# Kernel tuning notes

Measured on AMD Instinct MI355X. Metric: run time of the kernel, lower is better.

The kernel has to match this reference:

```python
import jax, jax.numpy as jnp
import numpy as np
from jax import lax

EPS = 1e-20
BN_EPS = 1e-5
ATTN_SCALE = 2.8284271247461903  # sqrt(d_l=8)
NS = (32, 32, 32, 10)
DS = (8, 8, 8, 16)


def squash(x):
    # Efficient-CapsNet squash: (1 - 1/(exp(||x||)+eps)) * x/(||x||+eps)
    norm = jnp.linalg.norm(x, axis=-1, keepdims=True)
    return (1.0 - 1.0 / (jnp.exp(norm) + EPS)) * (x / (norm + EPS))


def conv2d(x, w, b, stride, groups=1):
    y = lax.conv_general_dilated(
        x, w, window_strides=(stride, stride), padding='VALID',
        dimension_numbers=('NCHW', 'OIHW', 'NCHW'),
        feature_group_count=groups)
    return y + b[None, :, None, None]


def bn(x, g, b, m, v):
    inv = g / jnp.sqrt(v + BN_EPS)
    return x * inv[None, :, None, None] + (b - m * inv)[None, :, None, None]


def fccaps(U_l, W):
    # U_l: (b, n_l, d_l), W: (n_l, n_h, d_l, d_h)
    U_hat = jnp.einsum('bij,ikjl->bikl', U_l, W)          # (b, n_l, n_h, d_h)
    A = jnp.einsum('bikl,bhkl->bhik', U_hat, U_hat)        # (b, n_l, n_l, n_h)
    A_sum = jnp.sum(A, axis=-2)                            # (b, n_l, n_h)
    C = jax.nn.softmax(A_sum / ATTN_SCALE, axis=-1)        # (b, n_l, n_h)
    U_h = jnp.einsum('bikl,bik->bkl', U_hat, C)            # (b, n_h, d_h)
    return squash(U_h)


def setup_inputs() -> dict:
    key = jax.random.key(0)
    ks = jax.random.split(key, 8)
    B = 512
    x = jax.random.normal(ks[0], (B, 1, 39, 39), dtype=jnp.float32)
    conv1_w = jax.random.normal(ks[1], (128, 1, 3, 3), jnp.float32) * 0.2
    conv1_b = jnp.zeros((128,), jnp.float32)
    conv2_w = jax.random.normal(ks[2], (256, 128, 3, 3), jnp.float32) * 0.04
    conv2_b = jnp.zeros((256,), jnp.float32)
    conv3_w = jax.random.normal(ks[3], (256, 1, 9, 9), jnp.float32) * 0.1  # depthwise
    conv3_b = jnp.zeros((256,), jnp.float32)
    bn1_g = jnp.ones((128,), jnp.float32); bn1_b = jnp.zeros((128,), jnp.float32)
    bn1_m = jnp.zeros((128,), jnp.float32); bn1_v = jnp.ones((128,), jnp.float32)
    bn2_g = jnp.ones((256,), jnp.float32); bn2_b = jnp.zeros((256,), jnp.float32)
    bn2_m = jnp.zeros((256,), jnp.float32); bn2_v = jnp.ones((256,), jnp.float32)
    # capsule weights, kaiming-ish scale sqrt(2/fan_in) with fan_in = n_h*d_l*d_h
    def caps_w(k, n_l, n_h, d_l, d_h):
        std = np.sqrt(2.0 / (n_h * d_l * d_h))
        return jax.random.normal(k, (n_l, n_h, d_l, d_h), jnp.float32) * std
    W1 = caps_w(ks[4], NS[0], NS[1], DS[0], DS[1])
    W2 = caps_w(ks[5], NS[1], NS[2], DS[1], DS[2])
    W3 = caps_w(ks[6], NS[2], NS[3], DS[2], DS[3])
    return dict(x=x, conv1_w=conv1_w, conv1_b=conv1_b,
                bn1_g=bn1_g, bn1_b=bn1_b, bn1_m=bn1_m, bn1_v=bn1_v,
                conv2_w=conv2_w, conv2_b=conv2_b,
                bn2_g=bn2_g, bn2_b=bn2_b, bn2_m=bn2_m, bn2_v=bn2_v,
                conv3_w=conv3_w, conv3_b=conv3_b, W1=W1, W2=W2, W3=W3)


def reference(x, conv1_w, conv1_b, bn1_g, bn1_b, bn1_m, bn1_v,
              conv2_w, conv2_b, bn2_g, bn2_b, bn2_m, bn2_v,
              conv3_w, conv3_b, W1, W2, W3):
    h = jax.nn.relu(bn(conv2d(x, conv1_w, conv1_b, 2), bn1_g, bn1_b, bn1_m, bn1_v))
    h = jax.nn.relu(bn(conv2d(h, conv2_w, conv2_b, 2), bn2_g, bn2_b, bn2_m, bn2_v))
    h = conv2d(h, conv3_w, conv3_b, 1, groups=256)        # (B, 256, 1, 1)
    u = h.reshape(h.shape[0], NS[0], DS[0])                # (B, 32, 8)
    u = squash(u)
    for W in (W1, W2, W3):
        u = fccaps(u, W)
    return u  # (B, 10, 16)
```

## Files before the change

### kernel.cpp

```cpp
#include <hip/hip_runtime.h>


typedef __attribute__((ext_vector_type(8))) short short8;
typedef __attribute__((ext_vector_type(4))) float f32x4;

__device__ __forceinline__ ushort f2bf(float x) {
    uint u = __float_as_uint(x);
    return (ushort)((u + 0x7FFFu + ((u >> 16) & 1u)) >> 16);
}
__device__ __forceinline__ void bfsplit(float x, ushort& h, ushort& l) {
    h = f2bf(x);
    float hf = __uint_as_float(((uint)h) << 16);
    l = f2bf(x - hf);
}

__global__ __launch_bounds__(256) void k_prep(
    const float* __restrict__ w2, uint* __restrict__ Bt,
    const float* __restrict__ w3, float* __restrict__ w3T,
    const float* __restrict__ W1, const float* __restrict__ W2,
    const float* __restrict__ W3, float* __restrict__ Wr1,
    float* __restrict__ Wr2, float* __restrict__ Wr3) {
    __shared__ __align__(16) float wbuf[64 * 288];
    const int b = blockIdx.x, t = threadIdx.x;
    if (b < 144) {
        const int sidx = b >> 2, coq = b & 3;
        const int chunk = sidx / 9, tap = sidx - chunk * 9;
        const int co0 = coq * 64;
        for (int idx = t; idx < 4608; idx += 256) {
            const int n = idx / 72, q = idx - n * 72;
            ((float4*)wbuf)[n * 72 + q] =
                *(const float4*)(w2 + (size_t)(co0 + n) * 1152 + chunk * 288 + q * 4);
        }
        __syncthreads();
        const int n = t & 63, dg = (t >> 6) * 4;
        const int cot = coq >> 1, nn = ((coq & 1) * 64) + n;
        uint* dst = Bt + (size_t)(sidx * 2 + cot) * 4096;
#pragma unroll
        for (int dd = 0; dd < 4; ++dd) {
            const int d = dg + dd;
            const float x = wbuf[n * 288 + (2 * d) * 9 + tap];
            const float y = wbuf[n * 288 + (2 * d + 1) * 9 + tap];
            ushort xh, xl, yh, yl;
            bfsplit(x, xh, xl);
            bfsplit(y, yl == yl ? yh : yh, yl);
            bfsplit(y, yh, yl);
            dst[nn * 16 + d]        = (uint)xh | ((uint)yh << 16);
            dst[2048 + nn * 16 + d] = (uint)xl | ((uint)yl << 16);
        }
    } else if (b < 225) {
        const int p = b - 144;
        w3T[p * 256 + t] = w3[t * 81 + p];
    } else {
        const int bb = b - 225;
        const int layer = bb >> 5, blk = bb & 31;
        const float* src = layer == 0 ? W1 : (layer == 1 ? W2 : W3);
        float* dst = layer == 0 ? Wr1 : (layer == 1 ? Wr2 : Wr3);
        const int d_h = (layer == 2) ? 16 : 8;
        const int total = (layer == 2) ? 5120 : 8192;
        for (int idx = blk * 256 + t; idx < 8 * total; idx += 32 * 256) {
            const int j = idx / total, e = idx - j * total;
            const int ik = e / d_h, l = e - ik * d_h;
            dst[idx] = src[(ik * 8 + j) * d_h + l];
        }
    }
}

__global__ __launch_bounds__(256) void k_conv1(
    const float* __restrict__ x, const float* __restrict__ w,
    const float* __restrict__ bias, const float* __restrict__ g,
    const float* __restrict__ bb, const float* __restrict__ bm,
    const float* __restrict__ bv, ushort* __restrict__ h1) {
    __shared__ __align__(16) float xs[1521];
    __shared__ float wls[1152];
    __shared__ float2 scsh[128];
    const int b = blockIdx.x, t = threadIdx.x;
    const float* xb = x + (size_t)b * 1521;
    for (int i = t; i < 1521; i += 256) xs[i] = xb[i];
    for (int i = t; i < 1152; i += 256) wls[i] = w[i];
    if (t < 128) {
        const float inv = g[t] * rsqrtf(bv[t] + 1e-5f);
        scsh[t] = make_float2(inv, bias[t] * inv + bb[t] - bm[t] * inv);
    }
    __syncthreads();
    const int o = t & 15, pg = t >> 4;
    float wr[8][9];
#pragma unroll
    for (int j = 0; j < 8; ++j)
#pragma unroll
        for (int k = 0; k < 9; ++k) wr[j][k] = wls[(o * 8 + j) * 9 + k];
    float2 ss[8];
#pragma unroll
    for (int j = 0; j < 8; ++j) ss[j] = scsh[o * 8 + j];
    const int chunk = o >> 2, ol = o & 3;
    ushort* cb = h1 + (size_t)b * 92416 + chunk * 23104;
    for (int p = pg; p < 361; p += 16) {
        const int y = p / 19, xq = p - y * 19;
        const int base = y * 78 + xq * 2;
        const float x0 = xs[base],      x1 = xs[base + 1],  x2 = xs[base + 2];
        const float x3 = xs[base + 39], x4 = xs[base + 40], x5 = xs[base + 41];
        const float x6 = xs[base + 78], x7 = xs[base + 79], x8 = xs[base + 80];
        short8 hs, ls;
#pragma unroll
        for (int j = 0; j < 8; ++j) {
            const float acc = x0 * wr[j][0] + x1 * wr[j][1] + x2 * wr[j][2] +
                              x3 * wr[j][3] + x4 * wr[j][4] + x5 * wr[j][5] +
                              x6 * wr[j][6] + x7 * wr[j][7] + x8 * wr[j][8];
            const float v = fmaxf(fmaf(acc, ss[j].x, ss[j].y), 0.0f);
            ushort hh, lw;
            bfsplit(v, hh, lw);
            hs[j] = (short)hh;
            ls[j] = (short)lw;
        }
        if ((xq & 1) == 0) {
            const int pos = y * 10 + (xq >> 1);
            *(short8*)(cb + ol * 1520 + pos * 8)         = hs;
            *(short8*)(cb + 11552 + ol * 1520 + pos * 8) = ls;
        } else {
            const int pos = y * 9 + (xq >> 1);
            *(short8*)(cb + 6080 + ol * 1368 + pos * 8)  = hs;
            *(short8*)(cb + 17632 + ol * 1368 + pos * 8) = ls;
        }
    }
}

__global__ __launch_bounds__(256, 3) void k_conv2(
    const uint* __restrict__ h1u, const uint* __restrict__ Bt,
    const float* __restrict__ g,
    const float* __restrict__ bb, const float* __restrict__ bm,
    const float* __restrict__ bv, const float* __restrict__ bias,
    const float* __restrict__ w3T, float* __restrict__ Uws) {
    __shared__ __align__(16) uint raw[11552];
    __shared__ float ured[128];
    const int t = threadIdx.x;
    const int lane = t & 63, wave = t >> 6;
    const int ln15 = lane & 15, lq = lane >> 4;
    const int wm = (wave >> 1) * 48, wn = (wave & 1) * 64;
    const int gg = blockIdx.x;
    const int bi  = ((gg >> 4) << 3) | (gg & 7);
    const int cot = (gg >> 3) & 1;
    const int co0 = cot * 128;

    int PE[3], PO[3];
#pragma unroll
    for (int i = 0; i < 3; ++i) {
        const int m = wm + i * 16 + ln15;
        const int p = m < 81 ? m : 80;
        const int oh = p / 9, ow = p - oh * 9;
        PE[i] = lq * 760 + oh * 80 + ow * 4;
        PO[i] = 3040 + lq * 684 + oh * 72 + ow * 4;
    }
    int BRDg[4];
#pragma unroll
    for (int j = 0; j < 4; ++j) {
        const int n = wn + j * 16 + ln15;
        BRDg[j] = n * 16 + lq * 4;
    }

    f32x4 acc[3][4] = {};
    uint4 Bn[8];
    {
        const uint* bp = Bt + (size_t)cot * 4096;
#pragma unroll
        for (int j = 0; j < 4; ++j) {
            Bn[j]     = *(const uint4*)(bp + BRDg[j]);
            Bn[4 + j] = *(const uint4*)(bp + 2048 + BRDg[j]);
        }
    }

#pragma unroll
    for (int c = 0; c < 4; ++c) {
        __syncthreads();
        {
            const uint4* src = (const uint4*)(h1u + (size_t)(bi * 4 + c) * 11552);
            uint4* dst = (uint4*)raw;
            uint4 tmp[11];
#pragma unroll
            for (int k = 0; k < 11; ++k) tmp[k] = src[t + k * 256];
            const bool extra = (t < 72);
            uint4 te;
            if (extra) te = src[t + 11 * 256];
#pragma unroll
            for (int k = 0; k < 11; ++k) dst[t + k * 256] = tmp[k];
            if (extra) dst[t + 11 * 256] = te;
        }
        __syncthreads();
        short8 a_h[3];
#pragma unroll
        for (int i = 0; i < 3; ++i)
            a_h[i] = *reinterpret_cast<const short8*>(raw + PE[i]);
#pragma unroll
        for (int tap = 0; tap < 9; ++tap) {
            const int s = c * 9 + tap;
            uint4 Bc[8];
#pragma unroll
            for (int q = 0; q < 8; ++q) Bc[q] = Bn[q];
            if (s < 35) {
                const uint* bp = Bt + (size_t)((s + 1) * 2 + cot) * 4096;
#pragma unroll
                for (int j = 0; j < 4; ++j) {
                    Bn[j]     = *(const uint4*)(bp + BRDg[j]);
                    Bn[4 + j] = *(const uint4*)(bp + 2048 + BRDg[j]);
                }
            }
            const int kh = tap / 3, kw = tap - kh * 3;
            const int odd = kw & 1;
            const int sE = kh * 40 + (kw >> 1) * 4;
            const int sO = kh * 36;
            short8 a_l[3];
#pragma unroll
            for (int i = 0; i < 3; ++i) {
                const int addr = odd ? (PO[i] + sO) : (PE[i] + sE);
                a_l[i] = *reinterpret_cast<const short8*>(raw + addr + 5776);
            }
            short8 a_hn[3];
            if (tap < 8) {
                const int tap2 = tap + 1;
                const int kh2 = tap2 / 3, kw2 = tap2 - kh2 * 3;
                const int odd2 = kw2 & 1;
                const int sE2 = kh2 * 40 + (kw2 >> 1) * 4;
                const int sO2 = kh2 * 36;
#pragma unroll
                for (int i = 0; i < 3; ++i) {
                    const int addr2 = odd2 ? (PO[i] + sO2) : (PE[i] + sE2);
                    a_hn[i] = *reinterpret_cast<const short8*>(raw + addr2);
                }
            }
            short8 bh[4], bl[4];
#pragma unroll
            for (int j = 0; j < 4; ++j) {
                bh[j] = __builtin_bit_cast(short8, Bc[j]);
                bl[j] = __builtin_bit_cast(short8, Bc[4 + j]);
            }
#pragma unroll
            for (int i = 0; i < 3; ++i)
#pragma unroll
                for (int j = 0; j < 4; ++j)
                    acc[i][j] = __builtin_amdgcn_mfma_f32_16x16x32_bf16(a_h[i], bh[j], acc[i][j], 0, 0, 0);
#pragma unroll
            for (int i = 0; i < 3; ++i)
#pragma unroll
                for (int j = 0; j < 4; ++j)
                    acc[i][j] = __builtin_amdgcn_mfma_f32_16x16x32_bf16(a_h[i], bl[j], acc[i][j], 0, 0, 0);
#pragma unroll
            for (int i = 0; i < 3; ++i)
#pragma unroll
                for (int j = 0; j < 4; ++j)
                    acc[i][j] = __builtin_amdgcn_mfma_f32_16x16x32_bf16(a_l[i], bh[j], acc[i][j], 0, 0, 0);
            if (tap < 8) {
#pragma unroll
                for (int i = 0; i < 3; ++i) a_h[i] = a_hn[i];
            }
        }
    }

    float scj[4], shj[4];
#pragma unroll
    for (int j = 0; j < 4; ++j) {
        const int co = co0 + wn + j * 16 + ln15;
        const float inv = g[co] * rsqrtf(bv[co] + 1e-5f);
        scj[j] = inv;
        shj[j] = bias[co] * inv + bb[co] - bm[co] * inv;
    }
    float usum[4] = {0.f, 0.f, 0.f, 0.f};
#pragma unroll
    for (int i = 0; i < 3; ++i)
#pragma unroll
        for (int r = 0; r < 4; ++r) {
            const int m = wm + i * 16 + lq * 4 + r;
            if (m < 81) {
                const float* wrow = w3T + m * 256 + co0;
#pragma unroll
                for (int j = 0; j < 4; ++j) {
                    const int col = wn + j * 16 + ln15;
                    const float v = fmaxf(fmaf(acc[i][j][r], scj[j], shj[j]), 0.0f);
                    usum[j] = fmaf(v, wrow[col], usum[j]);
                }
            }
        }
#pragma unroll
    for (int j = 0; j < 4; ++j) {
        usum[j] += __shfl_xor(usum[j], 16);
        usum[j] += __shfl_xor(usum[j], 32);
    }
    if (lq == 0 && wm == 0) {
#pragma unroll
        for (int j = 0; j < 4; ++j) ured[(wn >> 6) * 64 + j * 16 + ln15] = usum[j];
    }
    __syncthreads();
    if (lq == 0 && wm == 48) {
#pragma unroll
        for (int j = 0; j < 4; ++j) {
            const int col = wn + j * 16 + ln15;
            Uws[(size_t)bi * 256 + co0 + col] =
                usum[j] + ured[(wn >> 6) * 64 + j * 16 + ln15];
        }
    }
}

__device__ __forceinline__ void fccaps_block(
    const int n_l, const int n_h, const int d_h, const float* __restrict__ Wr,
    float* U, float* Uh, float* Sv, float* Av, float* Cv, float* coefs,
    float* outU, const int t) {
    const int nkd = n_h * d_h;
    const int total = n_l * nkd;
    __syncthreads();
    for (int e = t; e < total; e += 256) {
        const int i = e / nkd;
        const float* up = U + i * 8;
        float acc = 0.0f;
#pragma unroll
        for (int j = 0; j < 8; ++j) acc += up[j] * Wr[j * total + e];
        Uh[e] = acc;
    }
    __syncthreads();
    for (int e = t; e < nkd; e += 256) {
        float acc = 0.0f;
        for (int i = 0; i < n_l; ++i) acc += Uh[i * nkd + e];
        Sv[e] = acc;
    }
    __syncthreads();
    for (int e = t; e < n_l * n_h; e += 256) {
        const int h = e / n_h, k = e - h * n_h;
        float acc = 0.0f;
        for (int l = 0; l < d_h; ++l)
            acc += Uh[h * nkd + k * d_h + l] * Sv[k * d_h + l];
        Av[e] = acc;
    }
    __syncthreads();
    {
        const int h = t >> 3, sub = t & 7;
        const float invs = 1.0f / 2.8284271247461903f;
        float mx = -1e30f;
        for (int k = sub; k < n_h; k += 8) mx = fmaxf(mx, Av[h * n_h + k]);
        mx = fmaxf(mx, __shfl_xor(mx, 1));
        mx = fmaxf(mx, __shfl_xor(mx, 2));
        mx = fmaxf(mx, __shfl_xor(mx, 4));
        float sum = 0.0f;
        for (int k = sub; k < n_h; k += 8) {
            const float ev = expf((Av[h * n_h + k] - mx) * invs);
            Cv[h * n_h + k] = ev;
            sum += ev;
        }
        sum += __shfl_xor(sum, 1);
        sum += __shfl_xor(sum, 2);
        sum += __shfl_xor(sum, 4);
        const float r = 1.0f / sum;
        for (int k = sub; k < n_h; k += 8) Cv[h * n_h + k] *= r;
    }
    __syncthreads();
    for (int e = t; e < nkd; e += 256) {
        const int k = e / d_h;
        float acc = 0.0f;
        for (int i = 0; i < n_l; ++i) acc += Uh[i * nkd + e] * Cv[i * n_h + k];
        Sv[e] = acc;
    }
    __syncthreads();
    if (t < n_h) {
        float ssq = 0.0f;
        for (int l = 0; l < d_h; ++l) { const float uv = Sv[t * d_h + l]; ssq += uv * uv; }
        const float n = sqrtf(ssq);
        coefs[t] = (1.0f - 1.0f / (expf(n) + 1e-20f)) / (n + 1e-20f);
    }
    __syncthreads();
    for (int e = t; e < nkd; e += 256) outU[e] = Sv[e] * coefs[e / d_h];
}

__global__ __launch_bounds__(256) void k_caps(
    const float* __restrict__ Uws, const float* __restrict__ b3,
    const float* __restrict__ Wr1, const float* __restrict__ Wr2,
    const float* __restrict__ Wr3, float* __restrict__ out) {
    __shared__ float U[256];
    __shared__ float Uh[8192];
    __shared__ float Sv[256];
    __shared__ float Av[1024];
    __shared__ float Cv[1024];
    __shared__ float coefs[32];
    const int b = blockIdx.x, t = threadIdx.x;
    U[t] = Uws[(size_t)b * 256 + t] + b3[t];
    __syncthreads();
    if (t < 32) {
        float ssq = 0.0f;
        for (int j = 0; j < 8; ++j) { const float uv = U[t * 8 + j]; ssq += uv * uv; }
        const float n = sqrtf(ssq);
        coefs[t] = (1.0f - 1.0f / (expf(n) + 1e-20f)) / (n + 1e-20f);
    }
    __syncthreads();
    U[t] *= coefs[t >> 3];
    fccaps_block(32, 32,  8, Wr1, U, Uh, Sv, Av, Cv, coefs, U, t);
    fccaps_block(32, 32,  8, Wr2, U, Uh, Sv, Av, Cv, coefs, U, t);
    fccaps_block(32, 10, 16, Wr3, U, Uh, Sv, Av, Cv, coefs, out + (size_t)b * 160, t);
}

extern "C" void kernel_launch(void* const* d_in, const int* in_sizes, int n_in,
                              void* d_out, int out_size, void* d_ws, size_t ws_size,
                              hipStream_t stream) {
    const float* x    = (const float*)d_in[0];
    const float* c1w  = (const float*)d_in[1];
    const float* c1b  = (const float*)d_in[2];
    const float* bn1g = (const float*)d_in[3];
    const float* bn1b = (const float*)d_in[4];
    const float* bn1m = (const float*)d_in[5];
    const float* bn1v = (const float*)d_in[6];
    const float* c2w  = (const float*)d_in[7];
    const float* c2b  = (const float*)d_in[8];
    const float* bn2g = (const float*)d_in[9];
    const float* bn2b = (const float*)d_in[10];
    const float* bn2m = (const float*)d_in[11];
    const float* bn2v = (const float*)d_in[12];
    const float* c3w  = (const float*)d_in[13];
    const float* c3b  = (const float*)d_in[14];
    const float* W1   = (const float*)d_in[15];
    const float* W2   = (const float*)d_in[16];
    const float* W3   = (const float*)d_in[17];
    float* out = (float*)d_out;
    uint*  wsu = (uint*)d_ws;
    float* wsf = (float*)d_ws;

    ushort* h1  = (ushort*)wsu;
    float*  Uws = wsf + 23658496;
    uint*   Bt  = wsu + 23789568;
    float*  w3T = wsf + 24084480;
    float*  Wr1 = wsf + 24105216;
    float*  Wr2 = wsf + 24170752;
    float*  Wr3 = wsf + 24236288;

    k_prep<<<dim3(321), 256, 0, stream>>>(c2w, Bt, c3w, w3T, W1, W2, W3,
                                          Wr1, Wr2, Wr3);
    k_conv1<<<dim3(512), 256, 0, stream>>>(x, c1w, c1b, bn1g, bn1b, bn1m, bn1v, h1);
    k_conv2<<<dim3(1024), 256, 0, stream>>>((const uint*)h1, Bt, bn2g, bn2b, bn2m, bn2v,
                                            c2b, w3T, Uws);
    k_caps<<<dim3(512), 256, 0, stream>>>(Uws, c3b, Wr1, Wr2, Wr3, out);
}
```

Measured before the change: 228.0 us.

## Fuse conv1 into conv2 kernel, recomputing conv1 per channel chunk in LDS

Removes the separate conv1 kernel and its large h1 intermediate in global memory. Each conv2 block now loads the input image into shared memory and computes the conv1+BN+ReLU bf16 split for each 32-channel chunk directly into the staging buffer. BN1 scale is folded into conv1 weights in the prep kernel. This trades a large global write and read for duplicated conv1 compute across the two output-channel blocks per image, and for B-tile prefetch that restarts at each chunk instead of running across chunks.

```diff
diff --git a/kernel.cpp b/kernel.cpp
--- a/kernel.cpp
+++ b/kernel.cpp
@@ -19,7 +19,11 @@
     const float* __restrict__ w3, float* __restrict__ w3T,
     const float* __restrict__ W1, const float* __restrict__ W2,
     const float* __restrict__ W3, float* __restrict__ Wr1,
-    float* __restrict__ Wr2, float* __restrict__ Wr3) {
+    float* __restrict__ Wr2, float* __restrict__ Wr3,
+    const float* __restrict__ c1w, const float* __restrict__ c1b,
+    const float* __restrict__ g1, const float* __restrict__ bb1,
+    const float* __restrict__ bm1, const float* __restrict__ bv1,
+    float* __restrict__ w1s, float* __restrict__ b1s) {
     __shared__ __align__(16) float wbuf[64 * 288];
     const int b = blockIdx.x, t = threadIdx.x;
     if (b < 144) {
@@ -42,7 +46,6 @@
             const float y = wbuf[n * 288 + (2 * d + 1) * 9 + tap];
             ushort xh, xl, yh, yl;
             bfsplit(x, xh, xl);
-            bfsplit(y, yl == yl ? yh : yh, yl);
             bfsplit(y, yh, yl);
             dst[nn * 16 + d]        = (uint)xh | ((uint)yh << 16);
             dst[2048 + nn * 16 + d] = (uint)xl | ((uint)yl << 16);
@@ -50,7 +53,7 @@
     } else if (b < 225) {
         const int p = b - 144;
         w3T[p * 256 + t] = w3[t * 81 + p];
-    } else {
+    } else if (b < 321) {
         const int bb = b - 225;
         const int layer = bb >> 5, blk = bb & 31;
         const float* src = layer == 0 ? W1 : (layer == 1 ? W2 : W3);
@@ -62,74 +65,28 @@
             const int ik = e / d_h, l = e - ik * d_h;
             dst[idx] = src[(ik * 8 + j) * d_h + l];
         }
-    }
-}
-
-__global__ __launch_bounds__(256) void k_conv1(
-    const float* __restrict__ x, const float* __restrict__ w,
-    const float* __restrict__ bias, const float* __restrict__ g,
-    const float* __restrict__ bb, const float* __restrict__ bm,
-    const float* __restrict__ bv, ushort* __restrict__ h1) {
-    __shared__ __align__(16) float xs[1521];
-    __shared__ float wls[1152];
-    __shared__ float2 scsh[128];
-    const int b = blockIdx.x, t = threadIdx.x;
-    const float* xb = x + (size_t)b * 1521;
-    for (int i = t; i < 1521; i += 256) xs[i] = xb[i];
-    for (int i = t; i < 1152; i += 256) wls[i] = w[i];
-    if (t < 128) {
-        const float inv = g[t] * rsqrtf(bv[t] + 1e-5f);
-        scsh[t] = make_float2(inv, bias[t] * inv + bb[t] - bm[t] * inv);
-    }
-    __syncthreads();
-    const int o = t & 15, pg = t >> 4;
-    float wr[8][9];
-#pragma unroll
-    for (int j = 0; j < 8; ++j)
-#pragma unroll
-        for (int k = 0; k < 9; ++k) wr[j][k] = wls[(o * 8 + j) * 9 + k];
-    float2 ss[8];
-#pragma unroll
-    for (int j = 0; j < 8; ++j) ss[j] = scsh[o * 8 + j];
-    const int chunk = o >> 2, ol = o & 3;
-    ushort* cb = h1 + (size_t)b * 92416 + chunk * 23104;
-    for (int p = pg; p < 361; p += 16) {
-        const int y = p / 19, xq = p - y * 19;
-        const int base = y * 78 + xq * 2;
-        const float x0 = xs[base],      x1 = xs[base + 1],  x2 = xs[base + 2];
-        const float x3 = xs[base + 39], x4 = xs[base + 40], x5 = xs[base + 41];
-        const float x6 = xs[base + 78], x7 = xs[base + 79], x8 = xs[base + 80];
-        short8 hs, ls;
-#pragma unroll
-        for (int j = 0; j < 8; ++j) {
-            const float acc = x0 * wr[j][0] + x1 * wr[j][1] + x2 * wr[j][2] +
-                              x3 * wr[j][3] + x4 * wr[j][4] + x5 * wr[j][5] +
-                              x6 * wr[j][6] + x7 * wr[j][7] + x8 * wr[j][8];
-            const float v = fmaxf(fmaf(acc, ss[j].x, ss[j].y), 0.0f);
-            ushort hh, lw;
-            bfsplit(v, hh, lw);
-            hs[j] = (short)hh;
-            ls[j] = (short)lw;
-        }
-        if ((xq & 1) == 0) {
-            const int pos = y * 10 + (xq >> 1);
-            *(short8*)(cb + ol * 1520 + pos * 8)         = hs;
-            *(short8*)(cb + 11552 + ol * 1520 + pos * 8) = ls;
-        } else {
-            const int pos = y * 9 + (xq >> 1);
-            *(short8*)(cb + 6080 + ol * 1368 + pos * 8)  = hs;
-            *(short8*)(cb + 17632 + ol * 1368 + pos * 8) = ls;
+    } else {
+        for (int i = t; i < 1152; i += 256) {
+            const int c = i / 9;
+            const float inv = g1[c] * rsqrtf(bv1[c] + 1e-5f);
+            w1s[i] = c1w[i] * inv;
+        }
+        if (t < 128) {
+            const float inv = g1[t] * rsqrtf(bv1[t] + 1e-5f);
+            b1s[t] = c1b[t] * inv + bb1[t] - bm1[t] * inv;
         }
     }
 }
 
 __global__ __launch_bounds__(256, 3) void k_conv2(
-    const uint* __restrict__ h1u, const uint* __restrict__ Bt,
+    const float* __restrict__ x, const float* __restrict__ w1s,
+    const float* __restrict__ b1s, const uint* __restrict__ Bt,
     const float* __restrict__ g,
     const float* __restrict__ bb, const float* __restrict__ bm,
     const float* __restrict__ bv, const float* __restrict__ bias,
     const float* __restrict__ w3T, float* __restrict__ Uws) {
     __shared__ __align__(16) uint raw[11552];
+    __shared__ __align__(16) float xsf[1521];
     __shared__ float ured[128];
     const int t = threadIdx.x;
     const int lane = t & 63, wave = t >> 6;
@@ -156,45 +113,82 @@
         BRDg[j] = n * 16 + lq * 4;
     }
 
+    {
+        const float* xb = x + (size_t)bi * 1521;
+        for (int i = t; i < 1521; i += 256) xsf[i] = xb[i];
+    }
+
     f32x4 acc[3][4] = {};
     uint4 Bn[8];
-    {
-        const uint* bp = Bt + (size_t)cot * 4096;
-#pragma unroll
-        for (int j = 0; j < 4; ++j) {
-            Bn[j]     = *(const uint4*)(bp + BRDg[j]);
-            Bn[4 + j] = *(const uint4*)(bp + 2048 + BRDg[j]);
-        }
-    }
-
-#pragma unroll
+
     for (int c = 0; c < 4; ++c) {
         __syncthreads();
         {
-            const uint4* src = (const uint4*)(h1u + (size_t)(bi * 4 + c) * 11552);
-            uint4* dst = (uint4*)raw;
-            uint4 tmp[11];
-#pragma unroll
-            for (int k = 0; k < 11; ++k) tmp[k] = src[t + k * 256];
-            const bool extra = (t < 72);
-            uint4 te;
-            if (extra) te = src[t + 11 * 256];
-#pragma unroll
-            for (int k = 0; k < 11; ++k) dst[t + k * 256] = tmp[k];
-            if (extra) dst[t + 11 * 256] = te;
+            const int o = wave;
+            const float* wp = w1s + (c * 32 + o * 8) * 9;
+            float wr[8][9];
+            float bs[8];
+#pragma unroll
+            for (int j = 0; j < 8; ++j) {
+#pragma unroll
+                for (int k = 0; k < 9; ++k) wr[j][k] = wp[j * 9 + k];
+                bs[j] = b1s[c * 32 + o * 8 + j];
+            }
+            ushort* stg = (ushort*)raw;
+#pragma unroll
+            for (int it = 0; it < 6; ++it) {
+                const int p = lane + 64 * it;
+                if (p < 361) {
+                    const int y = p / 19, xq = p - y * 19;
+                    const int base = y * 78 + xq * 2;
+                    const float x0 = xsf[base],      x1 = xsf[base + 1],  x2 = xsf[base + 2];
+                    const float x3 = xsf[base + 39], x4 = xsf[base + 40], x5 = xsf[base + 41];
+                    const float x6 = xsf[base + 78], x7 = xsf[base + 79], x8 = xsf[base + 80];
+                    short8 hs, ls;
+#pragma unroll
+                    for (int j = 0; j < 8; ++j) {
+                        const float a2 = bs[j] +
+                            x0 * wr[j][0] + x1 * wr[j][1] + x2 * wr[j][2] +
+                            x3 * wr[j][3] + x4 * wr[j][4] + x5 * wr[j][5] +
+                            x6 * wr[j][6] + x7 * wr[j][7] + x8 * wr[j][8];
+                        const float v = fmaxf(a2, 0.0f);
+                        ushort hh, lw;
+                        bfsplit(v, hh, lw);
+                        hs[j] = (short)hh;
+                        ls[j] = (short)lw;
+                    }
+                    if ((xq & 1) == 0) {
+                        const int pos = y * 10 + (xq >> 1);
+                        *(short8*)(stg + o * 1520 + pos * 8)         = hs;
+                        *(short8*)(stg + 11552 + o * 1520 + pos * 8) = ls;
+                    } else {
+                        const int pos = y * 9 + (xq >> 1);
+                        *(short8*)(stg + 6080 + o * 1368 + pos * 8)  = hs;
+                        *(short8*)(stg + 17632 + o * 1368 + pos * 8) = ls;
+                    }
+                }
+            }
         }
         __syncthreads();
+        {
+            const uint* bp = Bt + (size_t)(c * 18 + cot) * 4096;
+#pragma unroll
+            for (int j = 0; j < 4; ++j) {
+                Bn[j]     = *(const uint4*)(bp + BRDg[j]);
+                Bn[4 + j] = *(const uint4*)(bp + 2048 + BRDg[j]);
+            }
+        }
         short8 a_h[3];
 #pragma unroll
         for (int i = 0; i < 3; ++i)
             a_h[i] = *reinterpret_cast<const short8*>(raw + PE[i]);
 #pragma unroll
         for (int tap = 0; tap < 9; ++tap) {
-            const int s = c * 9 + tap;
             uint4 Bc[8];
 #pragma unroll
             for (int q = 0; q < 8; ++q) Bc[q] = Bn[q];
-            if (s < 35) {
+            if (tap < 8) {
+                const int s = c * 9 + tap;
                 const uint* bp = Bt + (size_t)((s + 1) * 2 + cot) * 4096;
 #pragma unroll
                 for (int j = 0; j < 4; ++j) {
@@ -416,18 +410,20 @@
     uint*  wsu = (uint*)d_ws;
     float* wsf = (float*)d_ws;
 
-    ushort* h1  = (ushort*)wsu;
-    float*  Uws = wsf + 23658496;
-    uint*   Bt  = wsu + 23789568;
-    float*  w3T = wsf + 24084480;
-    float*  Wr1 = wsf + 24105216;
-    float*  Wr2 = wsf + 24170752;
-    float*  Wr3 = wsf + 24236288;
-
-    k_prep<<<dim3(321), 256, 0, stream>>>(c2w, Bt, c3w, w3T, W1, W2, W3,
-                                          Wr1, Wr2, Wr3);
-    k_conv1<<<dim3(512), 256, 0, stream>>>(x, c1w, c1b, bn1g, bn1b, bn1m, bn1v, h1);
-    k_conv2<<<dim3(1024), 256, 0, stream>>>((const uint*)h1, Bt, bn2g, bn2b, bn2m, bn2v,
-                                            c2b, w3T, Uws);
+    float*  Uws = wsf;
+    uint*   Bt  = wsu + 131072;
+    float*  w3T = wsf + 425984;
+    float*  Wr1 = wsf + 446720;
+    float*  Wr2 = wsf + 512256;
+    float*  Wr3 = wsf + 577792;
+    float*  w1s = wsf + 618752;
+    float*  b1s = wsf + 619904;
+
+    k_prep<<<dim3(322), 256, 0, stream>>>(c2w, Bt, c3w, w3T, W1, W2, W3,
+                                          Wr1, Wr2, Wr3,
+                                          c1w, c1b, bn1g, bn1b, bn1m, bn1v,
+                                          w1s, b1s);
+    k_conv2<<<dim3(1024), 256, 0, stream>>>(x, w1s, b1s, Bt, bn2g, bn2b, bn2m,
+                                            bn2v, c2b, w3T, Uws);
     k_caps<<<dim3(512), 256, 0, stream>>>(Uws, c3b, Wr1, Wr2, Wr3, out);
 }
```

Result: slower. 261.2 us (+14.6%).
